# Optimization experiments

Measured on AMD Instinct MI355X. Metric: run time of the kernel, lower is better.

The kernel has to match this reference:

```python
import jax, jax.numpy as jnp
import numpy as np

N = 50000
E = 640000
D = 128
H = 512
LN_EPS = 1e-5


def setup_inputs() -> dict:
    key = jax.random.key(0)
    ks = jax.random.split(key, 6)
    x = jax.random.normal(ks[0], (N, D), dtype=jnp.float32)
    edge_index = jax.random.randint(ks[1], (2, E), 0, N, dtype=jnp.int64)
    edge_dist = jax.random.uniform(ks[2], (E,), dtype=jnp.float32)
    # true out-degrees of src so degree normalization is realistic
    degrees = jax.ops.segment_sum(jnp.ones((E,), jnp.float32), edge_index[0], num_segments=N)
    W1 = jax.random.normal(ks[3], (2 * D + 2, H), dtype=jnp.float32) * (1.0 / np.sqrt(2 * D + 2))
    b1 = jnp.zeros((H,), jnp.float32)
    W2 = jax.random.normal(ks[4], (H, D), dtype=jnp.float32) * (1.0 / np.sqrt(H))
    b2 = jnp.zeros((D,), jnp.float32)
    gamma = jnp.ones((D,), jnp.float32)
    beta = jnp.zeros((D,), jnp.float32)
    return {"x": x, "W1": W1, "b1": b1, "W2": W2, "b2": b2,
            "gamma": gamma, "beta": beta,
            "edge_index": edge_index, "edge_dist": edge_dist, "degrees": degrees}


def reference(x, W1, b1, W2, b2, gamma, beta, edge_index, edge_dist, degrees):
    n = x.shape[0]
    src, dst = edge_index[0], edge_index[1]
    # gather neighbor features, scatter-add into source nodes
    msg = x[dst]                                             # [E, D]
    agg = jax.ops.segment_sum(msg, src, num_segments=n)      # [N, D]
    deg = jnp.maximum(degrees, 1.0)                          # clamp_min(1.0)
    agg = agg / deg[:, None]
    dist_sum = jax.ops.segment_sum(edge_dist, src, num_segments=n)  # [N]
    mean_dist = dist_sum / deg                               # [N]
    feat = jnp.concatenate([x, agg, degrees[:, None], mean_dist[:, None]], axis=-1)  # [N, 2D+2]
    h = jax.nn.relu(feat @ W1 + b1)
    out = h @ W2 + b2
    y = x + out
    mu = jnp.mean(y, axis=-1, keepdims=True)
    var = jnp.var(y, axis=-1, keepdims=True)
    return (y - mu) / jnp.sqrt(var + LN_EPS) * gamma + beta
```

## Files before the change

kernel.cpp:

```cpp
#include <hip/hip_runtime.h>
#include <hip/hip_bf16.h>

#define NN 50000
#define EE 640000
#define LN_EPS 1e-5f
#define KD 272
#define KB 544
#define NBK2 782
#define CH 4096

typedef __bf16 bf16x8 __attribute__((ext_vector_type(8)));
typedef float f32x16 __attribute__((ext_vector_type(16)));

static __device__ __forceinline__ unsigned short f2bf(float f) {
    return __builtin_bit_cast(unsigned short, (__bf16)f);
}
static __device__ __forceinline__ float bflo(unsigned int u) {
    return __builtin_bit_cast(float, u << 16);
}
static __device__ __forceinline__ float bfhi(unsigned int u) {
    return __builtin_bit_cast(float, u & 0xffff0000u);
}

__global__ __launch_bounds__(256) void cast_x(const float* __restrict__ x,
                                              unsigned short* __restrict__ xbf) {
    int i = blockIdx.x * 256 + threadIdx.x;
    const float4* s = (const float4*)x + (size_t)i * 2;
    float4 a = s[0], b = s[1];
    unsigned short o[8] = { f2bf(a.x), f2bf(a.y), f2bf(a.z), f2bf(a.w),
                            f2bf(b.x), f2bf(b.y), f2bf(b.z), f2bf(b.w) };
    *(uint4*)(xbf + (size_t)i * 8) = *(const uint4*)o;
}

__global__ __launch_bounds__(256) void prep_weights(const float* __restrict__ W1,
                                                    const float* __restrict__ b1,
                                                    const float* __restrict__ W2,
                                                    unsigned short* __restrict__ W1Te,
                                                    unsigned short* __restrict__ W2T) {
    int b = blockIdx.x, tid = threadIdx.x;
    if (b < 512) {
        W1Te[(size_t)b * KD + tid] = f2bf(W1[(size_t)tid * 512 + b]);
        if (tid < 16) {
            float v = 0.f;
            if (tid == 0) v = W1[256 * 512 + b];
            else if (tid == 1) v = W1[257 * 512 + b];
            else if (tid == 2) v = b1[b];
            W1Te[(size_t)b * KD + 256 + tid] = f2bf(v);
        }
    } else {
        int c = b - 512;
        W2T[(size_t)c * 512 + tid]       = f2bf(W2[(size_t)tid * 128 + c]);
        W2T[(size_t)c * 512 + 256 + tid] = f2bf(W2[(size_t)(256 + tid) * 128 + c]);
    }
}

__global__ __launch_bounds__(256) void scanA(const float* __restrict__ degrees,
                                             int* __restrict__ blocksum) {
    __shared__ int wsum[4];
    int i = blockIdx.x * 256 + threadIdx.x;
    int v = (i < NN) ? (int)(degrees[i] + 0.5f) : 0;
    int s = v;
    for (int d = 1; d < 64; d <<= 1) s += __shfl_xor(s, d, 64);
    if ((threadIdx.x & 63) == 0) wsum[threadIdx.x >> 6] = s;
    __syncthreads();
    if (threadIdx.x == 0) blocksum[blockIdx.x] = wsum[0] + wsum[1] + wsum[2] + wsum[3];
}

__global__ __launch_bounds__(256) void scanB(const int* __restrict__ blocksum,
                                             int* __restrict__ blockoff, int nb) {
    __shared__ int wsum[4];
    int tid = threadIdx.x;
    int v = (tid < nb) ? blocksum[tid] : 0;
    int lane = tid & 63, wid = tid >> 6;
    int inc = v;
    for (int d = 1; d < 64; d <<= 1) { int t = __shfl_up(inc, d, 64); if (lane >= d) inc += t; }
    if (lane == 63) wsum[wid] = inc;
    __syncthreads();
    int add = 0;
    for (int w = 0; w < wid; w++) add += wsum[w];
    inc += add;
    if (tid < nb) blockoff[tid] = inc - v;
}

__global__ __launch_bounds__(256) void scanC(const float* __restrict__ degrees,
                                             const int* __restrict__ blockoff,
                                             int* __restrict__ start,
                                             int* __restrict__ gcur) {
    __shared__ int wsum[4];
    int tid = threadIdx.x;
    int i = blockIdx.x * 256 + tid;
    int v = (i < NN) ? (int)(degrees[i] + 0.5f) : 0;
    int lane = tid & 63, wid = tid >> 6;
    int inc = v;
    for (int d = 1; d < 64; d <<= 1) { int t = __shfl_up(inc, d, 64); if (lane >= d) inc += t; }
    if (lane == 63) wsum[wid] = inc;
    __syncthreads();
    int add = blockoff[blockIdx.x];
    for (int w = 0; w < wid; w++) add += wsum[w];
    int excl = add + inc - v;
    if (i < NN) {
        start[i] = excl;
        if ((i & 63) == 0) gcur[i >> 6] = excl;
    }
}

__global__ __launch_bounds__(256) void bin_kernel(const int* __restrict__ ei,
                                                  const float* __restrict__ edist,
                                                  int* __restrict__ gcur,
                                                  unsigned* __restrict__ recs1,
                                                  float* __restrict__ dist) {
    __shared__ int cnt[NBK2], off[NBK2], gb[NBK2], c2[NBK2];
    __shared__ int wsum[4];
    __shared__ unsigned stage[CH];
    __shared__ int gtg[CH];
    int tid = threadIdx.x, lane = tid & 63, wid = tid >> 6;
    int e0 = blockIdx.x * CH;
    int nval = EE - e0; if (nval > CH) nval = CH;

    for (int i = tid; i < NBK2; i += 256) { cnt[i] = 0; c2[i] = 0; }
    __syncthreads();
#pragma unroll
    for (int k = 0; k < CH / 256; k++) {
        int e = e0 + k * 256 + tid;
        if (e < EE) atomicAdd(&cnt[ei[e] >> 6], 1);
    }
    __syncthreads();
    {
        int v[4], s = 0;
#pragma unroll
        for (int j = 0; j < 4; j++) {
            int idx = tid * 4 + j;
            v[j] = (idx < NBK2) ? cnt[idx] : 0;
            s += v[j];
        }
        int inc = s;
        for (int d = 1; d < 64; d <<= 1) { int t = __shfl_up(inc, d, 64); if (lane >= d) inc += t; }
        if (lane == 63) wsum[wid] = inc;
        __syncthreads();
        int base = 0;
        for (int w = 0; w < wid; w++) base += wsum[w];
        int ex = base + inc - s;
#pragma unroll
        for (int j = 0; j < 4; j++) {
            int idx = tid * 4 + j;
            if (idx < NBK2) off[idx] = ex;
            ex += v[j];
        }
    }
    __syncthreads();
    for (int i = tid; i < NBK2; i += 256) {
        int c = cnt[i];
        gb[i] = c ? atomicAdd(&gcur[i], c) : 0;
    }
    __syncthreads();
#pragma unroll
    for (int k = 0; k < CH / 256; k++) {
        int e = e0 + k * 256 + tid;
        if (e < EE) {
            int s = ei[e];
            int d = ei[EE + e];
            atomicAdd(dist + s, edist[e]);
            int b = s >> 6;
            int p = atomicAdd(&c2[b], 1);
            int slot = off[b] + p;
            stage[slot] = (unsigned)d | ((unsigned)(s & 63) << 16);
            gtg[slot] = gb[b] + p;
        }
    }
    __syncthreads();
    for (int i = tid; i < nval; i += 256)
        recs1[gtg[i]] = stage[i];
}

__global__ __launch_bounds__(256) void subsort_kernel(const unsigned* __restrict__ recs1,
                                                      const int* __restrict__ start,
                                                      unsigned short* __restrict__ recs2) {
    __shared__ int cur[64];
    int bkt = blockIdx.x, tid = threadIdx.x;
    int bstart = start[bkt * 64];
    int bend = (bkt == NBK2 - 1) ? EE : start[(bkt + 1) * 64];
    if (tid < 64) {
        int node = bkt * 64 + tid;
        cur[tid] = (node < NN) ? start[node] : EE;
    }
    __syncthreads();
    for (int i = bstart + tid; i < bend; i += 256) {
        unsigned r = recs1[i];
        int p = atomicAdd(&cur[(r >> 16) & 63], 1);
        recs2[p] = (unsigned short)(r & 0xffffu);
    }
}

__global__ __launch_bounds__(256) void aggfeat_kernel(const unsigned short* __restrict__ xbf,
                                                      const int* __restrict__ start,
                                                      const float* __restrict__ degrees,
                                                      const unsigned short* __restrict__ recs2,
                                                      const float* __restrict__ dist,
                                                      unsigned short* __restrict__ featbf) {
    int tid = threadIdx.x;
    int node = blockIdx.x * 4 + (tid >> 6);
    int lane = tid & 63;
    if (node >= NN) return;
    int st = start[node];
    int cnt = (int)(degrees[node] + 0.5f);
    float a0 = 0.f, a1 = 0.f;
    for (int base = 0; base < cnt; base += 64) {
        int rem = cnt - base;
        int nv = rem < 64 ? rem : 64;
        int didx = (lane < nv) ? (int)recs2[st + base + lane] : 0;
        int j = 0;
        for (; j + 4 <= nv; j += 4) {
            int d0 = __shfl(didx, j,     64);
            int d1 = __shfl(didx, j + 1, 64);
            int d2 = __shfl(didx, j + 2, 64);
            int d3 = __shfl(didx, j + 3, 64);
            unsigned x0 = *(const unsigned*)(xbf + (size_t)d0 * 128 + lane * 2);
            unsigned x1 = *(const unsigned*)(xbf + (size_t)d1 * 128 + lane * 2);
            unsigned x2 = *(const unsigned*)(xbf + (size_t)d2 * 128 + lane * 2);
            unsigned x3 = *(const unsigned*)(xbf + (size_t)d3 * 128 + lane * 2);
            a0 += bflo(x0) + bflo(x1) + bflo(x2) + bflo(x3);
            a1 += bfhi(x0) + bfhi(x1) + bfhi(x2) + bfhi(x3);
        }
        for (; j < nv; j++) {
            int dj = __shfl(didx, j, 64);
            unsigned xv = *(const unsigned*)(xbf + (size_t)dj * 128 + lane * 2);
            a0 += bflo(xv);
            a1 += bfhi(xv);
        }
    }
    float dg = degrees[node];
    float degc = fmaxf(dg, 1.0f);
    float inv = 1.0f / degc;
    unsigned short* row = featbf + (size_t)node * KD;
    *(unsigned int*)(row + lane * 2) = *(const unsigned int*)(xbf + (size_t)node * 128 + lane * 2);
    unsigned short o2[2] = { f2bf(a0 * inv), f2bf(a1 * inv) };
    *(unsigned int*)(row + 128 + lane * 2) = *(const unsigned int*)o2;
    if (lane < 4) {
        unsigned short t4[4] = { 0, 0, 0, 0 };
        if (lane == 0) { t4[0] = f2bf(dg); t4[1] = f2bf(dist[node] * inv); t4[2] = f2bf(1.0f); }
        *(uint2*)(row + 256 + lane * 4) = *(const uint2*)t4;
    }
}

__global__ __launch_bounds__(256, 2) void fused_mlp_ln(const unsigned short* __restrict__ featbf,
                                                       const unsigned short* __restrict__ W1Te,
                                                       const unsigned short* __restrict__ W2T,
                                                       const float* __restrict__ x,
                                                       const float* __restrict__ b2,
                                                       const float* __restrict__ gamma,
                                                       const float* __restrict__ beta,
                                                       float* __restrict__ out) {
    __shared__ __align__(16) unsigned char lds[34816 + 16384];
    unsigned char* B1 = lds;
    unsigned char* B2 = lds + 34816;

    int tid = threadIdx.x;
    int wave = tid >> 6, lane = tid & 63;
    int ln = lane & 31, hi = lane >> 5;
    int rowbase = blockIdx.x * 128 + wave * 32;
    int gr = rowbase + ln;
    int xorv = (ln & 7) << 4;

    bf16x8 ffr[17];
    if (gr < NN) {
        const unsigned char* fp = (const unsigned char*)featbf + (size_t)gr * KB + hi * 16;
#pragma unroll
        for (int ks = 0; ks < 17; ks++)
            ffr[ks] = *(const bf16x8*)(fp + ks * 32);
    } else {
#pragma unroll
        for (int ks = 0; ks < 17; ks++) ffr[ks] = (bf16x8)(__bf16)0.0f;
    }

    f32x16 acc2[4] = {};

    for (int ct = 0; ct < 8; ct++) {
        const unsigned short* s1 = W1Te + (size_t)(ct * 64) * KD;
        for (int i = tid; i < 2048; i += 256) {
            int c = i >> 5, slot = i & 31;
            uint4 v = *(const uint4*)(s1 + c * KD + slot * 8);
            *(uint4*)(B1 + ((c * KB + slot * 16) ^ ((c & 7) << 4))) = v;
        }
        if (tid < 128) {
            int c = tid >> 1, half = tid & 1;
            uint4 v = *(const uint4*)(s1 + c * KD + 256 + half * 8);
            *(uint4*)(B1 + ((c * KB + 512 + half * 16) ^ ((c & 7) << 4))) = v;
        }
        const unsigned short* s2 = W2T + ct * 64;
        for (int i = tid; i < 1024; i += 256) {
            int c = i >> 3, s = i & 7;
            uint4 v = *(const uint4*)(s2 + (size_t)c * 512 + s * 8);
            *(uint4*)(B2 + ((c * 128 + s * 16) ^ ((c & 7) << 4))) = v;
        }
        __syncthreads();

        f32x16 acc1[2] = {};
#pragma unroll
        for (int ks = 0; ks < 17; ks++) {
#pragma unroll
            for (int t = 0; t < 2; t++) {
                int col = t * 32 + ln;
                bf16x8 af = *(const bf16x8*)(B1 + ((col * KB + ks * 32 + hi * 16) ^ xorv));
                acc1[t] = __builtin_amdgcn_mfma_f32_32x32x16_bf16(af, ffr[ks], acc1[t], 0, 0, 0);
            }
        }

        unsigned int dw[2][4][2];
#pragma unroll
        for (int t = 0; t < 2; t++)
#pragma unroll
            for (int g = 0; g < 4; g++)
#pragma unroll
                for (int i = 0; i < 2; i++) {
                    float lo = fmaxf(acc1[t][g * 4 + 2 * i], 0.f);
                    float hf = fmaxf(acc1[t][g * 4 + 2 * i + 1], 0.f);
                    dw[t][g][i] = (unsigned int)f2bf(lo) | ((unsigned int)f2bf(hf) << 16);
                }

#pragma unroll
        for (int t = 0; t < 2; t++)
#pragma unroll
            for (int w = 0; w < 2; w++) {
                int ks2 = t * 2 + w;
                unsigned int sL0 = dw[t][2 * w][0],     sL1 = dw[t][2 * w][1];
                unsigned int sH0 = dw[t][2 * w + 1][0], sH1 = dw[t][2 * w + 1][1];
                unsigned int send0 = hi ? sL0 : sH0;
                unsigned int send1 = hi ? sL1 : sH1;
                unsigned int r0 = (unsigned int)__shfl_xor((int)send0, 32, 64);
                unsigned int r1 = (unsigned int)__shfl_xor((int)send1, 32, 64);
                uint4 fd;
                fd.x = hi ? r0 : sL0;
                fd.y = hi ? r1 : sL1;
                fd.z = hi ? sH0 : r0;
                fd.w = hi ? sH1 : r1;
                bf16x8 hfr = __builtin_bit_cast(bf16x8, fd);
#pragma unroll
                for (int at = 0; at < 4; at++) {
                    int col2 = at * 32 + ln;
                    bf16x8 a2 = *(const bf16x8*)(B2 + ((col2 * 128 + ks2 * 32 + hi * 16) ^ xorv));
                    acc2[at] = __builtin_amdgcn_mfma_f32_32x32x16_bf16(a2, hfr, acc2[at], 0, 0, 0);
                }
            }
        __syncthreads();
    }

    bool rok = (gr < NN);
    float sum = 0.f, sq = 0.f;
#pragma unroll
    for (int at = 0; at < 4; at++)
#pragma unroll
        for (int g = 0; g < 4; g++) {
            int c0 = at * 32 + g * 8 + hi * 4;
            float4 bq = *(const float4*)(b2 + c0);
            float4 xq = rok ? *(const float4*)(x + (size_t)gr * 128 + c0) : make_float4(0, 0, 0, 0);
            float vb[4] = { bq.x, bq.y, bq.z, bq.w };
            float vx[4] = { xq.x, xq.y, xq.z, xq.w };
#pragma unroll
            for (int m = 0; m < 4; m++) {
                float v = acc2[at][g * 4 + m] + vb[m] + vx[m];
                acc2[at][g * 4 + m] = v;
                sum += v;
                sq += v * v;
            }
        }
    sum += __shfl_xor(sum, 32, 64);
    sq  += __shfl_xor(sq, 32, 64);
    float mu = sum * (1.0f / 128.0f);
    float var = sq * (1.0f / 128.0f) - mu * mu;
    float rs = rsqrtf(var + LN_EPS);
    if (rok) {
        float* orow = out + (size_t)gr * 128;
#pragma unroll
        for (int at = 0; at < 4; at++)
#pragma unroll
            for (int g = 0; g < 4; g++) {
                int c0 = at * 32 + g * 8 + hi * 4;
                float4 gq = *(const float4*)(gamma + c0);
                float4 be = *(const float4*)(beta + c0);
                float4 o;
                o.x = (acc2[at][g * 4 + 0] - mu) * rs * gq.x + be.x;
                o.y = (acc2[at][g * 4 + 1] - mu) * rs * gq.y + be.y;
                o.z = (acc2[at][g * 4 + 2] - mu) * rs * gq.z + be.z;
                o.w = (acc2[at][g * 4 + 3] - mu) * rs * gq.w + be.w;
                *(float4*)(orow + c0) = o;
            }
    }
}

extern "C" void kernel_launch(void* const* d_in, const int* in_sizes, int n_in,
                              void* d_out, int out_size, void* d_ws, size_t ws_size,
                              hipStream_t stream) {
    const float* x       = (const float*)d_in[0];
    const float* W1      = (const float*)d_in[1];
    const float* b1      = (const float*)d_in[2];
    const float* W2      = (const float*)d_in[3];
    const float* b2      = (const float*)d_in[4];
    const float* gamma   = (const float*)d_in[5];
    const float* beta    = (const float*)d_in[6];
    const int*   ei      = (const int*)d_in[7];
    const float* edist   = (const float*)d_in[8];
    const float* degrees = (const float*)d_in[9];
    float* out = (float*)d_out;

    char* ws = (char*)d_ws;
    size_t off = 0;
    auto alloc = [&](size_t bytes) {
        void* p = ws + off;
        off = (off + bytes + 255) & ~(size_t)255;
        return p;
    };
    unsigned* recs1         = (unsigned*)alloc((size_t)EE * 4);
    unsigned short* recs2   = (unsigned short*)alloc((size_t)EE * 2);
    int* start              = (int*)alloc((size_t)NN * 4);
    int* gcur               = (int*)alloc(NBK2 * 4);
    int* blocksum           = (int*)alloc(256 * 4);
    int* blockoff           = (int*)alloc(256 * 4);
    float* dist             = (float*)alloc((size_t)NN * 4);
    unsigned short* xbf     = (unsigned short*)alloc((size_t)NN * 128 * 2);
    unsigned short* featbf  = (unsigned short*)alloc((size_t)NN * KD * 2);
    unsigned short* W1Te    = (unsigned short*)alloc((size_t)512 * KD * 2);
    unsigned short* W2T     = (unsigned short*)alloc((size_t)128 * 512 * 2);

    const int NB = (NN + 255) / 256;

    hipMemsetAsync(dist, 0, (size_t)NN * 4, stream);
    cast_x<<<3125, 256, 0, stream>>>(x, xbf);
    prep_weights<<<640, 256, 0, stream>>>(W1, b1, W2, W1Te, W2T);
    scanA<<<NB, 256, 0, stream>>>(degrees, blocksum);
    scanB<<<1, 256, 0, stream>>>(blocksum, blockoff, NB);
    scanC<<<NB, 256, 0, stream>>>(degrees, blockoff, start, gcur);
    bin_kernel<<<(EE + CH - 1) / CH, 256, 0, stream>>>(ei, edist, gcur, recs1, dist);
    subsort_kernel<<<NBK2, 256, 0, stream>>>(recs1, start, recs2);
    aggfeat_kernel<<<(NN + 3) / 4, 256, 0, stream>>>(xbf, start, degrees, recs2, dist, featbf);
    fused_mlp_ln<<<(NN + 127) / 128, 256, 0, stream>>>(featbf, W1Te, W2T, x, b2, gamma, beta, out);
}
```

Measured before the change: 238.0 us.

## Double-buffer pre-laid weight image in LDS for fused MLP with smaller blocks

Weights are repacked once into a chunked image that already matches the MFMA fragment layout, so each chunk can be copied straight into LDS without swizzling. The fused MLP kernel now runs 128-thread blocks handling 64 rows each, walks H in 16 chunks of 32, and prefetches the next chunk into registers and then into a second LDS buffer while the current chunk computes. This overlaps weight loads with MFMA work and gives more blocks for occupancy. The cost is more per-block weight traffic, since each block covers fewer rows, and more registers held for the prefetch.

Result: slower. 359.4 us (+51.0%).

```diff
diff --git a/kernel.cpp b/kernel.cpp
--- a/kernel.cpp
+++ b/kernel.cpp
@@ -35,23 +35,28 @@
 __global__ __launch_bounds__(256) void prep_weights(const float* __restrict__ W1,
                                                     const float* __restrict__ b1,
                                                     const float* __restrict__ W2,
-                                                    unsigned short* __restrict__ W1Te,
-                                                    unsigned short* __restrict__ W2T) {
-    int b = blockIdx.x, tid = threadIdx.x;
-    if (b < 512) {
-        W1Te[(size_t)b * KD + tid] = f2bf(W1[(size_t)tid * 512 + b]);
-        if (tid < 16) {
-            float v = 0.f;
-            if (tid == 0) v = W1[256 * 512 + b];
-            else if (tid == 1) v = W1[257 * 512 + b];
-            else if (tid == 2) v = b1[b];
-            W1Te[(size_t)b * KD + 256 + tid] = f2bf(v);
-        }
+                                                    unsigned short* __restrict__ Wimg) {
+    int idx = blockIdx.x * 256 + threadIdx.x;
+    int ct = idx / 12800;
+    int r = idx - ct * 12800;
+    float v = 0.f;
+    if (r < 8704) {
+        int slot = r >> 8;
+        int c = (r >> 3) & 31;
+        int e = r & 7;
+        int k = slot * 8 + e;
+        int col = ct * 32 + c;
+        if (k < 258) v = W1[(size_t)k * 512 + col];
+        else if (k == 258) v = b1[col];
     } else {
-        int c = b - 512;
-        W2T[(size_t)c * 512 + tid]       = f2bf(W2[(size_t)tid * 128 + c]);
-        W2T[(size_t)c * 512 + 256 + tid] = f2bf(W2[(size_t)(256 + tid) * 128 + c]);
-    }
+        int r2 = r - 8704;
+        int slot = r2 >> 10;
+        int c2 = (r2 >> 3) & 127;
+        int e = r2 & 7;
+        int k = ct * 32 + slot * 8 + e;
+        v = W2[(size_t)k * 128 + c2];
+    }
+    Wimg[idx] = f2bf(v);
 }
 
 __global__ __launch_bounds__(256) void scanA(const float* __restrict__ degrees,
@@ -242,24 +247,20 @@
     }
 }
 
-__global__ __launch_bounds__(256, 2) void fused_mlp_ln(const unsigned short* __restrict__ featbf,
-                                                       const unsigned short* __restrict__ W1Te,
-                                                       const unsigned short* __restrict__ W2T,
+__global__ __launch_bounds__(128, 2) void fused_mlp_ln(const unsigned short* __restrict__ featbf,
+                                                       const unsigned short* __restrict__ Wimg,
                                                        const float* __restrict__ x,
                                                        const float* __restrict__ b2,
                                                        const float* __restrict__ gamma,
                                                        const float* __restrict__ beta,
                                                        float* __restrict__ out) {
-    __shared__ __align__(16) unsigned char lds[34816 + 16384];
-    unsigned char* B1 = lds;
-    unsigned char* B2 = lds + 34816;
+    __shared__ __align__(16) unsigned char lds[51200];
 
     int tid = threadIdx.x;
     int wave = tid >> 6, lane = tid & 63;
     int ln = lane & 31, hi = lane >> 5;
-    int rowbase = blockIdx.x * 128 + wave * 32;
+    int rowbase = blockIdx.x * 64 + wave * 32;
     int gr = rowbase + ln;
-    int xorv = (ln & 7) << 4;
 
     bf16x8 ffr[17];
     if (gr < NN) {
@@ -274,73 +275,83 @@
 
     f32x16 acc2[4] = {};
 
-    for (int ct = 0; ct < 8; ct++) {
-        const unsigned short* s1 = W1Te + (size_t)(ct * 64) * KD;
-        for (int i = tid; i < 2048; i += 256) {
-            int c = i >> 5, slot = i & 31;
-            uint4 v = *(const uint4*)(s1 + c * KD + slot * 8);
-            *(uint4*)(B1 + ((c * KB + slot * 16) ^ ((c & 7) << 4))) = v;
-        }
-        if (tid < 128) {
-            int c = tid >> 1, half = tid & 1;
-            uint4 v = *(const uint4*)(s1 + c * KD + 256 + half * 8);
-            *(uint4*)(B1 + ((c * KB + 512 + half * 16) ^ ((c & 7) << 4))) = v;
-        }
-        const unsigned short* s2 = W2T + ct * 64;
-        for (int i = tid; i < 1024; i += 256) {
-            int c = i >> 3, s = i & 7;
-            uint4 v = *(const uint4*)(s2 + (size_t)c * 512 + s * 8);
-            *(uint4*)(B2 + ((c * 128 + s * 16) ^ ((c & 7) << 4))) = v;
-        }
-        __syncthreads();
-
-        f32x16 acc1[2] = {};
+    const uint4* img = (const uint4*)Wimg;
+    uint4 pre[13];
+#pragma unroll
+    for (int j = 0; j < 13; j++) {
+        int idx = tid + j * 128;
+        if (idx < 1600) pre[j] = img[idx];
+    }
+    {
+        uint4* lb = (uint4*)lds;
+#pragma unroll
+        for (int j = 0; j < 13; j++) {
+            int idx = tid + j * 128;
+            if (idx < 1600) lb[idx] = pre[j];
+        }
+    }
+    __syncthreads();
+
+    for (int ct = 0; ct < 16; ct++) {
+        const unsigned char* cur = lds + (ct & 1) * 25600;
+        unsigned char* nxt = lds + ((ct + 1) & 1) * 25600;
+
+        if (ct < 15) {
+            const uint4* src = img + (ct + 1) * 1600;
+#pragma unroll
+            for (int j = 0; j < 13; j++) {
+                int idx = tid + j * 128;
+                if (idx < 1600) pre[j] = src[idx];
+            }
+        }
+
+        f32x16 acc1 = {};
 #pragma unroll
         for (int ks = 0; ks < 17; ks++) {
-#pragma unroll
-            for (int t = 0; t < 2; t++) {
-                int col = t * 32 + ln;
-                bf16x8 af = *(const bf16x8*)(B1 + ((col * KB + ks * 32 + hi * 16) ^ xorv));
-                acc1[t] = __builtin_amdgcn_mfma_f32_32x32x16_bf16(af, ffr[ks], acc1[t], 0, 0, 0);
-            }
-        }
-
-        unsigned int dw[2][4][2];
-#pragma unroll
-        for (int t = 0; t < 2; t++)
-#pragma unroll
-            for (int g = 0; g < 4; g++)
-#pragma unroll
-                for (int i = 0; i < 2; i++) {
-                    float lo = fmaxf(acc1[t][g * 4 + 2 * i], 0.f);
-                    float hf = fmaxf(acc1[t][g * 4 + 2 * i + 1], 0.f);
-                    dw[t][g][i] = (unsigned int)f2bf(lo) | ((unsigned int)f2bf(hf) << 16);
-                }
-
-#pragma unroll
-        for (int t = 0; t < 2; t++)
-#pragma unroll
-            for (int w = 0; w < 2; w++) {
-                int ks2 = t * 2 + w;
-                unsigned int sL0 = dw[t][2 * w][0],     sL1 = dw[t][2 * w][1];
-                unsigned int sH0 = dw[t][2 * w + 1][0], sH1 = dw[t][2 * w + 1][1];
-                unsigned int send0 = hi ? sL0 : sH0;
-                unsigned int send1 = hi ? sL1 : sH1;
-                unsigned int r0 = (unsigned int)__shfl_xor((int)send0, 32, 64);
-                unsigned int r1 = (unsigned int)__shfl_xor((int)send1, 32, 64);
-                uint4 fd;
-                fd.x = hi ? r0 : sL0;
-                fd.y = hi ? r1 : sL1;
-                fd.z = hi ? sH0 : r0;
-                fd.w = hi ? sH1 : r1;
-                bf16x8 hfr = __builtin_bit_cast(bf16x8, fd);
-#pragma unroll
-                for (int at = 0; at < 4; at++) {
-                    int col2 = at * 32 + ln;
-                    bf16x8 a2 = *(const bf16x8*)(B2 + ((col2 * 128 + ks2 * 32 + hi * 16) ^ xorv));
-                    acc2[at] = __builtin_amdgcn_mfma_f32_32x32x16_bf16(a2, hfr, acc2[at], 0, 0, 0);
-                }
-            }
+            bf16x8 af = *(const bf16x8*)(cur + (2 * ks + hi) * 512 + ln * 16);
+            acc1 = __builtin_amdgcn_mfma_f32_32x32x16_bf16(af, ffr[ks], acc1, 0, 0, 0);
+        }
+
+        unsigned int dw[4][2];
+#pragma unroll
+        for (int g = 0; g < 4; g++)
+#pragma unroll
+            for (int i = 0; i < 2; i++) {
+                float lo = fmaxf(acc1[g * 4 + 2 * i], 0.f);
+                float hf = fmaxf(acc1[g * 4 + 2 * i + 1], 0.f);
+                dw[g][i] = (unsigned int)f2bf(lo) | ((unsigned int)f2bf(hf) << 16);
+            }
+
+        const unsigned char* B2c = cur + 17408;
+#pragma unroll
+        for (int w = 0; w < 2; w++) {
+            unsigned int sL0 = dw[2 * w][0],     sL1 = dw[2 * w][1];
+            unsigned int sH0 = dw[2 * w + 1][0], sH1 = dw[2 * w + 1][1];
+            unsigned int send0 = hi ? sL0 : sH0;
+            unsigned int send1 = hi ? sL1 : sH1;
+            unsigned int r0 = (unsigned int)__shfl_xor((int)send0, 32, 64);
+            unsigned int r1 = (unsigned int)__shfl_xor((int)send1, 32, 64);
+            uint4 fd;
+            fd.x = hi ? r0 : sL0;
+            fd.y = hi ? r1 : sL1;
+            fd.z = hi ? sH0 : r0;
+            fd.w = hi ? sH1 : r1;
+            bf16x8 hfr = __builtin_bit_cast(bf16x8, fd);
+#pragma unroll
+            for (int at = 0; at < 4; at++) {
+                bf16x8 a2 = *(const bf16x8*)(B2c + (2 * w + hi) * 2048 + (at * 32 + ln) * 16);
+                acc2[at] = __builtin_amdgcn_mfma_f32_32x32x16_bf16(a2, hfr, acc2[at], 0, 0, 0);
+            }
+        }
+
+        if (ct < 15) {
+            uint4* lb = (uint4*)nxt;
+#pragma unroll
+            for (int j = 0; j < 13; j++) {
+                int idx = tid + j * 128;
+                if (idx < 1600) lb[idx] = pre[j];
+            }
+        }
         __syncthreads();
     }
 
@@ -418,19 +429,18 @@
     float* dist             = (float*)alloc((size_t)NN * 4);
     unsigned short* xbf     = (unsigned short*)alloc((size_t)NN * 128 * 2);
     unsigned short* featbf  = (unsigned short*)alloc((size_t)NN * KD * 2);
-    unsigned short* W1Te    = (unsigned short*)alloc((size_t)512 * KD * 2);
-    unsigned short* W2T     = (unsigned short*)alloc((size_t)128 * 512 * 2);
+    unsigned short* Wimg    = (unsigned short*)alloc((size_t)204800 * 2);
 
     const int NB = (NN + 255) / 256;
 
     hipMemsetAsync(dist, 0, (size_t)NN * 4, stream);
     cast_x<<<3125, 256, 0, stream>>>(x, xbf);
-    prep_weights<<<640, 256, 0, stream>>>(W1, b1, W2, W1Te, W2T);
+    prep_weights<<<800, 256, 0, stream>>>(W1, b1, W2, Wimg);
     scanA<<<NB, 256, 0, stream>>>(degrees, blocksum);
     scanB<<<1, 256, 0, stream>>>(blocksum, blockoff, NB);
     scanC<<<NB, 256, 0, stream>>>(degrees, blockoff, start, gcur);
     bin_kernel<<<(EE + CH - 1) / CH, 256, 0, stream>>>(ei, edist, gcur, recs1, dist);
     subsort_kernel<<<NBK2, 256, 0, stream>>>(recs1, start, recs2);
     aggfeat_kernel<<<(NN + 3) / 4, 256, 0, stream>>>(xbf, start, degrees, recs2, dist, featbf);
-    fused_mlp_ln<<<(NN + 127) / 128, 256, 0, stream>>>(featbf, W1Te, W2T, x, b2, gamma, beta, out);
-}
+    fused_mlp_ln<<<(NN + 63) / 64, 128, 0, stream>>>(featbf, Wimg, x, b2, gamma, beta, out);
+}
```
